# Kernel tuning notes

Measured on AMD Instinct MI355X. Metric: run time of the kernel, lower is better.

Reference implementation:

```python
import jax, jax.numpy as jnp
import numpy as np

B, S, D, H, FFN = 4, 1024, 1024, 16, 4096
DH = D // H
EPS = 1e-5
NEG = -1e20


def _layer_norm(t, g, b):
    m = jnp.mean(t, axis=-1, keepdims=True)
    v = jnp.mean((t - m) ** 2, axis=-1, keepdims=True)
    return (t - m) / jnp.sqrt(v + EPS) * g + b


def setup_inputs() -> dict:
    key = jax.random.key(0)
    ks = jax.random.split(key, 16)
    std_attn = np.sqrt(2.0 / (D + D)).astype(np.float32)  # xavier normal
    lim1 = np.sqrt(6.0 / (D + FFN)).astype(np.float32)    # xavier uniform
    inp = {
        'tensor': jax.random.normal(ks[0], (B, S, D), jnp.float32),
        'mask': jnp.ones((B, S), jnp.int32),
        'wq': jax.random.normal(ks[1], (D, D), jnp.float32) * std_attn,
        'bq': jnp.zeros((D,), jnp.float32),
        'wk': jax.random.normal(ks[2], (D, D), jnp.float32) * std_attn,
        'bk': jnp.zeros((D,), jnp.float32),
        'wv': jax.random.normal(ks[3], (D, D), jnp.float32) * std_attn,
        'bv': jnp.zeros((D,), jnp.float32),
        'wo': jax.random.normal(ks[4], (D, D), jnp.float32) * std_attn,
        'bo': jnp.zeros((D,), jnp.float32),
        'ln1_g': jnp.ones((D,), jnp.float32),
        'ln1_b': jnp.zeros((D,), jnp.float32),
        'w1': jax.random.uniform(ks[5], (FFN, D), jnp.float32, -lim1, lim1),
        'b1': jnp.zeros((FFN,), jnp.float32),
        'w2': jax.random.uniform(ks[6], (D, FFN), jnp.float32, -lim1, lim1),
        'b2': jnp.zeros((D,), jnp.float32),
        'ln2_g': jnp.ones((D,), jnp.float32),
        'ln2_b': jnp.zeros((D,), jnp.float32),
    }
    return inp


def reference(tensor, mask, wq, bq, wk, bk, wv, bv, wo, bo,
              ln1_g, ln1_b, w1, b1, w2, b2, ln2_g, ln2_b):
    x = tensor
    scale = jnp.sqrt(jnp.float32(DH))
    # QKV projections -> [B, S, H, DH]
    q = (x @ wq.T + bq).reshape(B, S, H, DH)
    k = (x @ wk.T + bk).reshape(B, S, H, DH)
    v = (x @ wv.T + bv).reshape(B, S, H, DH)
    # scores [B, H, Sq, Sk]
    scores = jnp.einsum('bqhd,bkhd->bhqk', q / scale, k)
    blocked = (mask == 0)[:, None, None, :]  # True -> block
    scores = jnp.where(blocked, NEG, scores)
    attn = jax.nn.softmax(scores.astype(jnp.float32), axis=-1).astype(x.dtype)
    ctx = jnp.einsum('bhqk,bkhd->bqhd', attn, v).reshape(B, S, D)
    attn_out = ctx @ wo.T + bo
    # post-LN (variant='aiayn')
    t = _layer_norm(x + attn_out, ln1_g, ln1_b)
    ffn = jax.nn.relu(t @ w1.T + b1) @ w2.T + b2
    t = _layer_norm(t + ffn, ln2_g, ln2_b)
    t = t * mask[:, :, None].astype(t.dtype)
    return t
```

## Files before the change

kernel.cpp:

```cpp
#include <hip/hip_runtime.h>

typedef __bf16 bf16x8 __attribute__((ext_vector_type(8)));
typedef __bf16 bf16x4 __attribute__((ext_vector_type(4)));
typedef float f32x4 __attribute__((ext_vector_type(4)));
typedef float f32x16 __attribute__((ext_vector_type(16)));

#define BB 4
#define SS 1024
#define DD 1024
#define HH 16
#define DHH 64
#define FFN 4096

__device__ __forceinline__ void gload_lds16(const void* g, void* lds) {
  __builtin_amdgcn_global_load_lds(
      (const __attribute__((address_space(1))) unsigned int*)g,
      (__attribute__((address_space(3))) unsigned int*)lds, 16, 0, 0);
}

__global__ __launch_bounds__(256) void cvt_all_kernel(
    const float* __restrict__ x, const float* __restrict__ wq, const float* __restrict__ wk,
    const float* __restrict__ wv, const float* __restrict__ wo, const float* __restrict__ w1,
    const float* __restrict__ w2, __bf16* __restrict__ xb, __bf16* __restrict__ wqkvb,
    __bf16* __restrict__ wob, __bf16* __restrict__ w1b, __bf16* __restrict__ w2b)
{
  int i = blockIdx.x * 256 + threadIdx.x;
  const float* src; __bf16* dst; int off;
  if (i < 524288)       { src = x;  dst = xb;              off = i; }
  else if (i < 655360)  { src = wq; dst = wqkvb;           off = i - 524288; }
  else if (i < 786432)  { src = wk; dst = wqkvb + 1048576; off = i - 655360; }
  else if (i < 917504)  { src = wv; dst = wqkvb + 2097152; off = i - 786432; }
  else if (i < 1048576) { src = wo; dst = wob;             off = i - 917504; }
  else if (i < 1572864) { src = w1; dst = w1b;             off = i - 1048576; }
  else                  { src = w2; dst = w2b;             off = i - 1572864; }
  float4 a = *(const float4*)(src + off * 8);
  float4 b = *(const float4*)(src + off * 8 + 4);
  bf16x8 v;
  v[0] = (__bf16)a.x; v[1] = (__bf16)a.y; v[2] = (__bf16)a.z; v[3] = (__bf16)a.w;
  v[4] = (__bf16)b.x; v[5] = (__bf16)b.y; v[6] = (__bf16)b.z; v[7] = (__bf16)b.w;
  *(bf16x8*)(dst + off * 8) = v;
}

template<int MODE>
__global__ __launch_bounds__(256, 2) void gemm_bt(
    const __bf16* __restrict__ A, const __bf16* __restrict__ Bw,
    const float* __restrict__ bias, const float* __restrict__ bias1, const float* __restrict__ bias2,
    const float* __restrict__ res, void* __restrict__ outp, void* __restrict__ out1,
    int M, int N, int K, int kLen, float scale)
{
  __shared__ __bf16 As[2][128 * 32];
  __shared__ __bf16 Bs[2][128 * 32];
  const int tid = threadIdx.x;
  const int wid = tid >> 6;
  const int lane = tid & 63;
  const int lr = lane & 15;
  const int lg = lane >> 4;

  const int gx = gridDim.x;
  const int nwg = gx * gridDim.y;
  const int wg = blockIdx.y * gx + blockIdx.x;
  const int swz = (wg & 7) * (nwg >> 3) + (wg >> 3);
  const int bm = (swz / gx) * 128;
  const int bn = (swz % gx) * 128;

  const int wm = (wid >> 1) * 64;
  const int wn = (wid & 1) * 64;

  int kBeg = 0, nk = K >> 5;
  if constexpr (MODE == 5) { kBeg = blockIdx.z * kLen; nk = kLen >> 5; }

  const int off = tid * 16;
  const int srow = off >> 6;
  const int scol = (off & 63) >> 1;
  const __bf16* gA0 = A + (size_t)(bm + srow) * K + kBeg + scol;
  const __bf16* gA1 = A + (size_t)(bm + 64 + srow) * K + kBeg + scol;
  const __bf16* gB0 = Bw + (size_t)(bn + srow) * K + kBeg + scol;
  const __bf16* gB1 = Bw + (size_t)(bn + 64 + srow) * K + kBeg + scol;
  char* lA = (char*)&As[0][0] + wid * 1024;
  char* lB = (char*)&Bs[0][0] + wid * 1024;

  f32x4 acc[4][4] = {};

#define STAGE(buf, kk) do { \
    gload_lds16(gA0 + (kk), lA + (buf) * 8192); \
    gload_lds16(gA1 + (kk), lA + (buf) * 8192 + 4096); \
    gload_lds16(gB0 + (kk), lB + (buf) * 8192); \
    gload_lds16(gB1 + (kk), lB + (buf) * 8192 + 4096); \
  } while (0)

  STAGE(0, 0);
  __syncthreads();
  for (int t = 0; t < nk; ++t) {
    const int cur = t & 1;
    if (t + 1 < nk) STAGE(cur ^ 1, (t + 1) << 5);
    bf16x8 af[4], bv[4];
#pragma unroll
    for (int i = 0; i < 4; ++i)
      af[i] = *(const bf16x8*)&As[cur][(wm + i * 16 + lr) * 32 + lg * 8];
#pragma unroll
    for (int i = 0; i < 4; ++i)
      bv[i] = *(const bf16x8*)&Bs[cur][(wn + i * 16 + lr) * 32 + lg * 8];
#pragma unroll
    for (int i = 0; i < 4; ++i)
#pragma unroll
      for (int j = 0; j < 4; ++j)
        acc[i][j] = __builtin_amdgcn_mfma_f32_16x16x32_bf16(af[i], bv[j], acc[i][j], 0, 0, 0);
    __syncthreads();
  }
#undef STAGE

#pragma unroll
  for (int i = 0; i < 4; ++i) {
#pragma unroll
    for (int j = 0; j < 4; ++j) {
#pragma unroll
      for (int r = 0; r < 4; ++r) {
        int row = bm + wm + i * 16 + lg * 4 + r;
        int col = bn + wn + j * 16 + lr;
        float v = acc[i][j][r];
        if constexpr (MODE == 2) {
          size_t idx = (size_t)row * N + col;
          ((float*)outp)[idx] = v + bias[col] + res[idx];
        } else if constexpr (MODE == 3) {
          float t2 = v + bias[col];
          ((__bf16*)outp)[(size_t)row * N + col] = (__bf16)fmaxf(t2, 0.f);
        } else if constexpr (MODE == 4) {
          int region = col >> 10;
          int col_ = col & 1023;
          int b_ = row >> 10, s_ = row & 1023;
          int h_ = col_ >> 6, d_ = col_ & 63;
          if (region == 0) {
            float v2 = (v + bias[col_]) * scale;
            ((__bf16*)outp)[(((size_t)(b_ * HH + h_) * SS) + s_) * DHH + d_] = (__bf16)v2;
          } else if (region == 1) {
            float v2 = v + bias1[col_];
            ((__bf16*)out1)[(((size_t)(b_ * HH + h_) * SS) + s_) * DHH + d_] = (__bf16)v2;
          } else {
            float v2 = v + bias2[col_];
            ((__bf16*)res)[(((size_t)(b_ * HH + h_) * DHH) + d_) * SS + s_] = (__bf16)v2;
          }
        } else {
          float* dst = blockIdx.z ? (float*)out1 : (float*)outp;
          dst[(size_t)row * N + col] = v;
        }
      }
    }
  }
}

__global__ __launch_bounds__(256, 2) void attn_kernel(
    const __bf16* __restrict__ q, const __bf16* __restrict__ k,
    const __bf16* __restrict__ vt, const int* __restrict__ mask,
    __bf16* __restrict__ ctx)
{
  const int nwg = gridDim.x;
  const int wg = blockIdx.x;
  const int swzb = (wg & 7) * (nwg >> 3) + (wg >> 3);
  const int bh = swzb >> 3;
  const int qb = (swzb & 7) << 7;
  const int b = bh >> 4;

  const int tid = threadIdx.x, wid = tid >> 6, lane = tid & 63;
  const int ln = lane & 31, hi = lane >> 5;

  __shared__ __bf16 Kt[2][64 * 64];
  __shared__ __bf16 Vt[2][64 * 64];
  __shared__ __bf16 Pt[4][32 * 64];
  __shared__ float mmulLds[SS];

  {
    const int* mrow = mask + b * SS;
    int c = tid * 4;
    float4 mm;
    mm.x = (float)(mrow[c + 0] != 0);
    mm.y = (float)(mrow[c + 1] != 0);
    mm.z = (float)(mrow[c + 2] != 0);
    mm.w = (float)(mrow[c + 3] != 0);
    ((float4*)mmulLds)[tid] = mm;
  }

  const __bf16* qh = q + (size_t)bh * SS * DHH;
  const __bf16* kh = k + (size_t)bh * SS * DHH;
  const __bf16* vh = vt + (size_t)bh * DHH * SS;

  const int qw = qb + wid * 32;
  bf16x8 qf[4];
#pragma unroll
  for (int s = 0; s < 4; ++s)
    qf[s] = *(const bf16x8*)&qh[(size_t)(qw + ln) * DHH + s * 16 + hi * 8];

  const int srow = tid >> 3;
  const int ps = tid & 7;
  const int sw0 = (srow ^ (srow >> 3)) & 7;
  const int r1 = srow + 32;
  const int sw1 = (r1 ^ (r1 >> 3)) & 7;
  const __bf16* kS0 = kh + (size_t)srow * DHH + ((ps ^ sw0) * 8);
  const __bf16* kS1 = kh + (size_t)r1 * DHH + ((ps ^ sw1) * 8);
  const __bf16* vS0 = vh + (size_t)srow * SS + ((ps ^ sw0) * 8);
  const __bf16* vS1 = vh + (size_t)r1 * SS + ((ps ^ sw1) * 8);

#define ASTAGE(bufi, kb_) do { \
    gload_lds16(kS0 + (size_t)(kb_) * DHH, (char*)&Kt[bufi][0] + wid * 1024); \
    gload_lds16(kS1 + (size_t)(kb_) * DHH, (char*)&Kt[bufi][0] + wid * 1024 + 4096); \
    gload_lds16(vS0 + (kb_), (char*)&Vt[bufi][0] + wid * 1024); \
    gload_lds16(vS1 + (kb_), (char*)&Vt[bufi][0] + wid * 1024 + 4096); \
  } while (0)

  char* Pw = (char*)&Pt[wid][0];
  const int swA = (ln ^ (ln >> 3)) & 7;
  const int swB = swA ^ 4;

  f32x16 o0 = {}, o1 = {};
  float l[16];
#pragma unroll
  for (int r = 0; r < 16; ++r) l[r] = 0.f;

  ASTAGE(0, 0);
  __syncthreads();

#pragma unroll 1
  for (int t = 0; t < SS / 64; ++t) {
    const int cur = t & 1;
    const int kb = t * 64;
    if (t + 1 < SS / 64) ASTAGE(cur ^ 1, kb + 64);

    const char* Kc = (const char*)&Kt[cur][0];
    const char* Vc = (const char*)&Vt[cur][0];

    f32x16 sc0 = {}, sc1 = {};
#pragma unroll
    for (int s = 0; s < 4; ++s) {
      bf16x8 kb0 = *(const bf16x8*)(Kc + ln * 128 + (((s * 2 + hi) ^ swA) << 4));
      bf16x8 kb1 = *(const bf16x8*)(Kc + (32 + ln) * 128 + (((s * 2 + hi) ^ swB) << 4));
      sc0 = __builtin_amdgcn_mfma_f32_32x32x16_bf16(qf[s], kb0, sc0, 0, 0, 0);
      sc1 = __builtin_amdgcn_mfma_f32_32x32x16_bf16(qf[s], kb1, sc1, 0, 0, 0);
    }

    float mm0 = mmulLds[kb + ln];
    float mm1 = mmulLds[kb + 32 + ln];
#pragma unroll
    for (int r = 0; r < 16; ++r) {
      float p0 = exp2f(sc0[r] - 23.0831207f) * mm0;
      float p1 = exp2f(sc1[r] - 23.0831207f) * mm1;
      l[r] += p0 + p1;
      int qrow = (r & 3) + 8 * (r >> 2) + 4 * hi;
      int swq = (qrow ^ (qrow >> 3)) & 7;
      *(__bf16*)(Pw + qrow * 128 + ((((ln >> 3) + 0) ^ swq) << 4) + (ln & 7) * 2) = (__bf16)p0;
      *(__bf16*)(Pw + qrow * 128 + ((((ln >> 3) + 4) ^ swq) << 4) + (ln & 7) * 2) = (__bf16)p1;
    }

#pragma unroll
    for (int ks = 0; ks < 4; ++ks) {
      bf16x8 pa = *(const bf16x8*)(Pw + ln * 128 + (((ks * 2 + hi) ^ swA) << 4));
      bf16x8 vb0 = *(const bf16x8*)(Vc + ln * 128 + (((ks * 2 + hi) ^ swA) << 4));
      bf16x8 vb1 = *(const bf16x8*)(Vc + (32 + ln) * 128 + (((ks * 2 + hi) ^ swB) << 4));
      o0 = __builtin_amdgcn_mfma_f32_32x32x16_bf16(pa, vb0, o0, 0, 0, 0);
      o1 = __builtin_amdgcn_mfma_f32_32x32x16_bf16(pa, vb1, o1, 0, 0, 0);
    }
    __syncthreads();
  }
#undef ASTAGE

#pragma unroll
  for (int r = 0; r < 16; ++r) {
#pragma unroll
    for (int off = 1; off < 32; off <<= 1) l[r] += __shfl_xor(l[r], off);
  }

#pragma unroll
  for (int r = 0; r < 16; ++r) {
    float inv = l[r] > 0.f ? 1.f / l[r] : 0.f;
    int qrow = (r & 3) + 8 * (r >> 2) + 4 * hi;
    size_t base = ((size_t)b * SS + qw + qrow) * DD + (size_t)(bh & 15) * DHH;
    ctx[base + ln] = (__bf16)(o0[r] * inv);
    ctx[base + 32 + ln] = (__bf16)(o1[r] * inv);
  }
}

__global__ __launch_bounds__(256) void ln_kernel(
    const float* __restrict__ in, const float* __restrict__ g, const float* __restrict__ b,
    float* __restrict__ out32, __bf16* __restrict__ out16)
{
  int row = blockIdx.x;
  int tid = threadIdx.x;
  int wid = tid >> 6, lane = tid & 63;
  float4 v = ((const float4*)(in + (size_t)row * DD))[tid];
  float s = v.x + v.y + v.z + v.w;
  float sq = v.x * v.x + v.y * v.y + v.z * v.z + v.w * v.w;
#pragma unroll
  for (int o = 1; o < 64; o <<= 1) { s += __shfl_xor(s, o); sq += __shfl_xor(sq, o); }
  __shared__ float red[8];
  if (lane == 0) { red[wid] = s; red[4 + wid] = sq; }
  __syncthreads();
  s = red[0] + red[1] + red[2] + red[3];
  sq = red[4] + red[5] + red[6] + red[7];
  float mean = s * (1.f / DD);
  float var = sq * (1.f / DD) - mean * mean;
  float rstd = rsqrtf(var + 1e-5f);
  float4 gg = ((const float4*)g)[tid];
  float4 bb = ((const float4*)b)[tid];
  float4 o;
  o.x = (v.x - mean) * rstd * gg.x + bb.x;
  o.y = (v.y - mean) * rstd * gg.y + bb.y;
  o.z = (v.z - mean) * rstd * gg.z + bb.z;
  o.w = (v.w - mean) * rstd * gg.w + bb.w;
  if (out32) ((float4*)(out32 + (size_t)row * DD))[tid] = o;
  if (out16) {
    bf16x4 w;
    w[0] = (__bf16)o.x; w[1] = (__bf16)o.y; w[2] = (__bf16)o.z; w[3] = (__bf16)o.w;
    *(bf16x4*)(out16 + (size_t)row * DD + tid * 4) = w;
  }
}

__global__ __launch_bounds__(256) void ln2_fused_kernel(
    const float* __restrict__ p0, const float* __restrict__ p1, const float* __restrict__ bias,
    const float* __restrict__ res, const float* __restrict__ g, const float* __restrict__ b,
    const int* __restrict__ mask, float* __restrict__ out)
{
  int row = blockIdx.x;
  int tid = threadIdx.x;
  int wid = tid >> 6, lane = tid & 63;
  size_t base = (size_t)row * DD;
  float4 a0 = ((const float4*)(p0 + base))[tid];
  float4 a1 = ((const float4*)(p1 + base))[tid];
  float4 rr = ((const float4*)(res + base))[tid];
  float4 bs = ((const float4*)bias)[tid];
  float4 v;
  v.x = a0.x + a1.x + rr.x + bs.x;
  v.y = a0.y + a1.y + rr.y + bs.y;
  v.z = a0.z + a1.z + rr.z + bs.z;
  v.w = a0.w + a1.w + rr.w + bs.w;
  float s = v.x + v.y + v.z + v.w;
  float sq = v.x * v.x + v.y * v.y + v.z * v.z + v.w * v.w;
#pragma unroll
  for (int o = 1; o < 64; o <<= 1) { s += __shfl_xor(s, o); sq += __shfl_xor(sq, o); }
  __shared__ float red[8];
  if (lane == 0) { red[wid] = s; red[4 + wid] = sq; }
  __syncthreads();
  s = red[0] + red[1] + red[2] + red[3];
  sq = red[4] + red[5] + red[6] + red[7];
  float mean = s * (1.f / DD);
  float var = sq * (1.f / DD) - mean * mean;
  float rstd = rsqrtf(var + 1e-5f);
  float4 gg = ((const float4*)g)[tid];
  float4 bb = ((const float4*)b)[tid];
  float mk = (float)mask[row];
  float4 o;
  o.x = ((v.x - mean) * rstd * gg.x + bb.x) * mk;
  o.y = ((v.y - mean) * rstd * gg.y + bb.y) * mk;
  o.z = ((v.z - mean) * rstd * gg.z + bb.z) * mk;
  o.w = ((v.w - mean) * rstd * gg.w + bb.w) * mk;
  ((float4*)(out + base))[tid] = o;
}

extern "C" void kernel_launch(void* const* d_in, const int* in_sizes, int n_in,
                              void* d_out, int out_size, void* d_ws, size_t ws_size,
                              hipStream_t stream) {
  const float* x    = (const float*)d_in[0];
  const int*  mask  = (const int*)d_in[1];
  const float* wq   = (const float*)d_in[2];
  const float* bq   = (const float*)d_in[3];
  const float* wk   = (const float*)d_in[4];
  const float* bk   = (const float*)d_in[5];
  const float* wv   = (const float*)d_in[6];
  const float* bv   = (const float*)d_in[7];
  const float* wo   = (const float*)d_in[8];
  const float* bo   = (const float*)d_in[9];
  const float* ln1g = (const float*)d_in[10];
  const float* ln1b = (const float*)d_in[11];
  const float* w1   = (const float*)d_in[12];
  const float* b1   = (const float*)d_in[13];
  const float* w2   = (const float*)d_in[14];
  const float* b2   = (const float*)d_in[15];
  const float* ln2g = (const float*)d_in[16];
  const float* ln2b = (const float*)d_in[17];
  float* out = (float*)d_out;
  char* ws = (char*)d_ws;

  __bf16* xb    = (__bf16*)(ws + 0);
  __bf16* wqkvb = (__bf16*)(ws + 8388608);
  __bf16* wob   = (__bf16*)(ws + 14680064);
  __bf16* w1b   = (__bf16*)(ws + 16777216);
  __bf16* w2b   = (__bf16*)(ws + 25165824);
  __bf16* qbuf  = (__bf16*)(ws + 33554432);
  __bf16* kbuf  = (__bf16*)(ws + 41943040);
  __bf16* vtbf  = (__bf16*)(ws + 50331648);
  __bf16* ctxb  = (__bf16*)(ws + 58720256);
  __bf16* hb    = (__bf16*)(ws + 33554432);
  float*  r1    = (float*)(ws + 67108864);
  float*  t32   = (float*)(ws + 83886080);
  __bf16* tb    = (__bf16*)(ws + 100663296);
  float*  p0    = r1;
  float*  p1    = (float*)(ws + 0);

  const int MSD = BB * SS;

  cvt_all_kernel<<<8192, 256, 0, stream>>>(x, wq, wk, wv, wo, w1, w2, xb, wqkvb, wob, w1b, w2b);

  gemm_bt<4><<<dim3(24, 32), 256, 0, stream>>>(xb, wqkvb, bq, bk, bv, (const float*)vtbf,
                                               qbuf, kbuf, MSD, 3072, DD, 0, 0.18033688f);

  attn_kernel<<<BB * HH * (SS / 128), 256, 0, stream>>>(qbuf, kbuf, vtbf, mask, ctxb);

  gemm_bt<2><<<dim3(8, 32), 256, 0, stream>>>(ctxb, wob, bo, nullptr, nullptr, x,
                                              r1, nullptr, MSD, DD, DD, 0, 1.0f);
  ln_kernel<<<MSD, 256, 0, stream>>>(r1, ln1g, ln1b, t32, tb);

  gemm_bt<3><<<dim3(32, 32), 256, 0, stream>>>(tb, w1b, b1, nullptr, nullptr, nullptr,
                                               hb, nullptr, MSD, FFN, DD, 0, 1.0f);
  gemm_bt<5><<<dim3(8, 32, 2), 256, 0, stream>>>(hb, w2b, nullptr, nullptr, nullptr, nullptr,
                                                 p0, p1, MSD, DD, FFN, 2048, 1.0f);
  ln2_fused_kernel<<<MSD, 256, 0, stream>>>(p0, p1, b2, t32, ln2g, ln2b, mask, out);
}
```

Before: 235.8 us.

## Add 4-stage pipelined 256-wide GEMM with swizzled LDS for QKV and FFN

```diff
diff --git a/kernel.cpp b/kernel.cpp
--- a/kernel.cpp
+++ b/kernel.cpp
@@ -41,87 +41,100 @@
   *(bf16x8*)(dst + off * 8) = v;
 }
 
-template<int MODE>
-__global__ __launch_bounds__(256, 2) void gemm_bt(
+template<int BM, int MODE>
+__global__ __launch_bounds__(512, 2) void gemm_pipe(
     const __bf16* __restrict__ A, const __bf16* __restrict__ Bw,
-    const float* __restrict__ bias, const float* __restrict__ bias1, const float* __restrict__ bias2,
-    const float* __restrict__ res, void* __restrict__ outp, void* __restrict__ out1,
+    const float* __restrict__ bias, const float* __restrict__ bias1,
+    const float* __restrict__ bias2, const float* __restrict__ res,
+    void* __restrict__ outp, void* __restrict__ out1,
     int M, int N, int K, int kLen, float scale)
 {
-  __shared__ __bf16 As[2][128 * 32];
-  __shared__ __bf16 Bs[2][128 * 32];
+  constexpr int MREP = BM / 32;
+  constexpr int ASLOT = BM * 64;
+  constexpr int BSLOT = 16384;
+  __shared__ char As[4 * ASLOT];
+  __shared__ char Bs[4 * BSLOT];
+
   const int tid = threadIdx.x;
-  const int wid = tid >> 6;
-  const int lane = tid & 63;
-  const int lr = lane & 15;
-  const int lg = lane >> 4;
+  const int wid = tid >> 6, lane = tid & 63;
+  const int lr = lane & 15, lg = lane >> 4;
+  const int wm = wid >> 2, wn = wid & 3;
 
   const int gx = gridDim.x;
   const int nwg = gx * gridDim.y;
   const int wg = blockIdx.y * gx + blockIdx.x;
   const int swz = (wg & 7) * (nwg >> 3) + (wg >> 3);
-  const int bm = (swz / gx) * 128;
-  const int bn = (swz % gx) * 128;
-
-  const int wm = (wid >> 1) * 64;
-  const int wn = (wid & 1) * 64;
-
-  int kBeg = 0, nk = K >> 5;
-  if constexpr (MODE == 5) { kBeg = blockIdx.z * kLen; nk = kLen >> 5; }
-
-  const int off = tid * 16;
-  const int srow = off >> 6;
-  const int scol = (off & 63) >> 1;
+  const int bm = (swz / gx) * BM;
+  const int bn = (swz % gx) * 256;
+
+  int kBeg = 0, KK = K;
+  if constexpr (MODE == 5) { kBeg = blockIdx.z * kLen; KK = kLen; }
+  const int NK = KK >> 5;
+
+  const int srow = tid >> 2;
+  const int scol = (((tid & 3) ^ ((srow >> 1) & 3)) << 3);
   const __bf16* gA0 = A + (size_t)(bm + srow) * K + kBeg + scol;
-  const __bf16* gA1 = A + (size_t)(bm + 64 + srow) * K + kBeg + scol;
+  const __bf16* gA1 = A + (size_t)(bm + 128 + srow) * K + kBeg + scol;
   const __bf16* gB0 = Bw + (size_t)(bn + srow) * K + kBeg + scol;
-  const __bf16* gB1 = Bw + (size_t)(bn + 64 + srow) * K + kBeg + scol;
-  char* lA = (char*)&As[0][0] + wid * 1024;
-  char* lB = (char*)&Bs[0][0] + wid * 1024;
-
-  f32x4 acc[4][4] = {};
-
-#define STAGE(buf, kk) do { \
-    gload_lds16(gA0 + (kk), lA + (buf) * 8192); \
-    gload_lds16(gA1 + (kk), lA + (buf) * 8192 + 4096); \
-    gload_lds16(gB0 + (kk), lB + (buf) * 8192); \
-    gload_lds16(gB1 + (kk), lB + (buf) * 8192 + 4096); \
+  const __bf16* gB1 = Bw + (size_t)(bn + 128 + srow) * K + kBeg + scol;
+  char* lA = As + wid * 1024;
+  char* lB = Bs + wid * 1024;
+
+  f32x4 acc[MREP][4] = {};
+
+#define STG(sI, kt) do { const int kk_ = (kt) << 5; \
+    gload_lds16(gA0 + kk_, lA + (sI) * ASLOT); \
+    if constexpr (BM == 256) gload_lds16(gA1 + kk_, lA + (sI) * ASLOT + 8192); \
+    gload_lds16(gB0 + kk_, lB + (sI) * BSLOT); \
+    gload_lds16(gB1 + kk_, lB + (sI) * BSLOT + 8192); \
   } while (0)
 
-  STAGE(0, 0);
-  __syncthreads();
-  for (int t = 0; t < nk; ++t) {
-    const int cur = t & 1;
-    if (t + 1 < nk) STAGE(cur ^ 1, (t + 1) << 5);
-    bf16x8 af[4], bv[4];
-#pragma unroll
-    for (int i = 0; i < 4; ++i)
-      af[i] = *(const bf16x8*)&As[cur][(wm + i * 16 + lr) * 32 + lg * 8];
-#pragma unroll
-    for (int i = 0; i < 4; ++i)
-      bv[i] = *(const bf16x8*)&Bs[cur][(wn + i * 16 + lr) * 32 + lg * 8];
-#pragma unroll
-    for (int i = 0; i < 4; ++i)
+  STG(0, 0); STG(1, 1); STG(2, 2);
+
+  const int swzb = (lg ^ ((lr >> 1) & 3)) << 4;
+
+#pragma unroll 1
+  for (int t = 0; t < NK; ++t) {
+    if constexpr (BM == 256)
+      asm volatile("s_waitcnt vmcnt(8)" ::: "memory");
+    else
+      asm volatile("s_waitcnt vmcnt(6)" ::: "memory");
+    __builtin_amdgcn_s_barrier();
+    __builtin_amdgcn_sched_barrier(0);
+    {
+      const int kt = (t + 3 < NK) ? (t + 3) : (NK - 1);
+      STG((t + 3) & 3, kt);
+    }
+    const char* Ac = As + (t & 3) * ASLOT;
+    const char* Bc = Bs + (t & 3) * BSLOT;
+    bf16x8 af[MREP], bf[4];
+#pragma unroll
+    for (int i = 0; i < MREP; ++i)
+      af[i] = *(const bf16x8*)(Ac + (wm * (BM / 2) + i * 16 + lr) * 64 + swzb);
+#pragma unroll
+    for (int j = 0; j < 4; ++j)
+      bf[j] = *(const bf16x8*)(Bc + (wn * 64 + j * 16 + lr) * 64 + swzb);
+    __builtin_amdgcn_s_setprio(1);
+#pragma unroll
+    for (int i = 0; i < MREP; ++i)
 #pragma unroll
       for (int j = 0; j < 4; ++j)
-        acc[i][j] = __builtin_amdgcn_mfma_f32_16x16x32_bf16(af[i], bv[j], acc[i][j], 0, 0, 0);
-    __syncthreads();
-  }
-#undef STAGE
-
-#pragma unroll
-  for (int i = 0; i < 4; ++i) {
+        acc[i][j] = __builtin_amdgcn_mfma_f32_16x16x32_bf16(af[i], bf[j], acc[i][j], 0, 0, 0);
+    __builtin_amdgcn_s_setprio(0);
+  }
+#undef STG
+  asm volatile("s_waitcnt vmcnt(0)" ::: "memory");
+
+#pragma unroll
+  for (int i = 0; i < MREP; ++i) {
 #pragma unroll
     for (int j = 0; j < 4; ++j) {
 #pragma unroll
       for (int r = 0; r < 4; ++r) {
-        int row = bm + wm + i * 16 + lg * 4 + r;
-        int col = bn + wn + j * 16 + lr;
+        int row = bm + wm * (BM / 2) + i * 16 + lg * 4 + r;
+        int col = bn + wn * 64 + j * 16 + lr;
         float v = acc[i][j][r];
-        if constexpr (MODE == 2) {
-          size_t idx = (size_t)row * N + col;
-          ((float*)outp)[idx] = v + bias[col] + res[idx];
-        } else if constexpr (MODE == 3) {
+        if constexpr (MODE == 3) {
           float t2 = v + bias[col];
           ((__bf16*)outp)[(size_t)row * N + col] = (__bf16)fmaxf(t2, 0.f);
         } else if constexpr (MODE == 4) {
@@ -148,6 +161,89 @@
   }
 }
 
+template<int MODE>
+__global__ __launch_bounds__(256, 2) void gemm_bt(
+    const __bf16* __restrict__ A, const __bf16* __restrict__ Bw,
+    const float* __restrict__ bias, const float* __restrict__ res,
+    void* __restrict__ outp, int M, int N, int K, float scale)
+{
+  __shared__ __bf16 As[2][128 * 32];
+  __shared__ __bf16 Bs[2][128 * 32];
+  const int tid = threadIdx.x;
+  const int wid = tid >> 6;
+  const int lane = tid & 63;
+  const int lr = lane & 15;
+  const int lg = lane >> 4;
+
+  const int gx = gridDim.x;
+  const int nwg = gx * gridDim.y;
+  const int wg = blockIdx.y * gx + blockIdx.x;
+  const int swz = (wg & 7) * (nwg >> 3) + (wg >> 3);
+  const int bm = (swz / gx) * 128;
+  const int bn = (swz % gx) * 128;
+
+  const int wm = (wid >> 1) * 64;
+  const int wn = (wid & 1) * 64;
+
+  const int off = tid * 16;
+  const int srow = off >> 6;
+  const int scol = (off & 63) >> 1;
+  const __bf16* gA0 = A + (size_t)(bm + srow) * K + scol;
+  const __bf16* gA1 = A + (size_t)(bm + 64 + srow) * K + scol;
+  const __bf16* gB0 = Bw + (size_t)(bn + srow) * K + scol;
+  const __bf16* gB1 = Bw + (size_t)(bn + 64 + srow) * K + scol;
+  char* lA = (char*)&As[0][0] + wid * 1024;
+  char* lB = (char*)&Bs[0][0] + wid * 1024;
+
+  f32x4 acc[4][4] = {};
+
+#define STAGE(buf, kk) do { \
+    gload_lds16(gA0 + (kk), lA + (buf) * 8192); \
+    gload_lds16(gA1 + (kk), lA + (buf) * 8192 + 4096); \
+    gload_lds16(gB0 + (kk), lB + (buf) * 8192); \
+    gload_lds16(gB1 + (kk), lB + (buf) * 8192 + 4096); \
+  } while (0)
+
+  STAGE(0, 0);
+  __syncthreads();
+  const int nk = K >> 5;
+  for (int t = 0; t < nk; ++t) {
+    const int cur = t & 1;
+    if (t + 1 < nk) STAGE(cur ^ 1, (t + 1) << 5);
+    bf16x8 af[4], bv[4];
+#pragma unroll
+    for (int i = 0; i < 4; ++i)
+      af[i] = *(const bf16x8*)&As[cur][(wm + i * 16 + lr) * 32 + lg * 8];
+#pragma unroll
+    for (int i = 0; i < 4; ++i)
+      bv[i] = *(const bf16x8*)&Bs[cur][(wn + i * 16 + lr) * 32 + lg * 8];
+#pragma unroll
+    for (int i = 0; i < 4; ++i)
+#pragma unroll
+      for (int j = 0; j < 4; ++j)
+        acc[i][j] = __builtin_amdgcn_mfma_f32_16x16x32_bf16(af[i], bv[j], acc[i][j], 0, 0, 0);
+    __syncthreads();
+  }
+#undef STAGE
+
+#pragma unroll
+  for (int i = 0; i < 4; ++i) {
+#pragma unroll
+    for (int j = 0; j < 4; ++j) {
+#pragma unroll
+      for (int r = 0; r < 4; ++r) {
+        int row = bm + wm + i * 16 + lg * 4 + r;
+        int col = bn + wn + j * 16 + lr;
+        float v = acc[i][j][r];
+        if constexpr (MODE == 2) {
+          size_t idx = (size_t)row * N + col;
+          ((float*)outp)[idx] = v + bias[col] + res[idx];
+        }
+      }
+    }
+  }
+}
+
 __global__ __launch_bounds__(256, 2) void attn_kernel(
     const __bf16* __restrict__ q, const __bf16* __restrict__ k,
     const __bf16* __restrict__ vt, const int* __restrict__ mask,
@@ -397,18 +493,19 @@
 
   cvt_all_kernel<<<8192, 256, 0, stream>>>(x, wq, wk, wv, wo, w1, w2, xb, wqkvb, wob, w1b, w2b);
 
-  gemm_bt<4><<<dim3(24, 32), 256, 0, stream>>>(xb, wqkvb, bq, bk, bv, (const float*)vtbf,
-                                               qbuf, kbuf, MSD, 3072, DD, 0, 0.18033688f);
+  gemm_pipe<256, 4><<<dim3(12, 16), 512, 0, stream>>>(
+      xb, wqkvb, bq, bk, bv, (const float*)vtbf, qbuf, kbuf, MSD, 3072, DD, 0, 0.18033688f);
 
   attn_kernel<<<BB * HH * (SS / 128), 256, 0, stream>>>(qbuf, kbuf, vtbf, mask, ctxb);
 
-  gemm_bt<2><<<dim3(8, 32), 256, 0, stream>>>(ctxb, wob, bo, nullptr, nullptr, x,
-                                              r1, nullptr, MSD, DD, DD, 0, 1.0f);
+  gemm_bt<2><<<dim3(8, 32), 256, 0, stream>>>(ctxb, wob, bo, x, r1, MSD, DD, DD, 1.0f);
   ln_kernel<<<MSD, 256, 0, stream>>>(r1, ln1g, ln1b, t32, tb);
 
-  gemm_bt<3><<<dim3(32, 32), 256, 0, stream>>>(tb, w1b, b1, nullptr, nullptr, nullptr,
-                                               hb, nullptr, MSD, FFN, DD, 0, 1.0f);
-  gemm_bt<5><<<dim3(8, 32, 2), 256, 0, stream>>>(hb, w2b, nullptr, nullptr, nullptr, nullptr,
-                                                 p0, p1, MSD, DD, FFN, 2048, 1.0f);
+  gemm_pipe<256, 3><<<dim3(16, 16), 512, 0, stream>>>(
+      tb, w1b, b1, nullptr, nullptr, nullptr, hb, nullptr, MSD, FFN, DD, 0, 1.0f);
+
+  gemm_pipe<128, 5><<<dim3(4, 32, 2), 512, 0, stream>>>(
+      hb, w2b, nullptr, nullptr, nullptr, nullptr, p0, p1, MSD, DD, FFN, 2048, 1.0f);
+
   ln2_fused_kernel<<<MSD, 256, 0, stream>>>(p0, p1, b2, t32, ln2g, ln2b, mask, out);
 }
```

Measured after the change: 289.3 us. +22.7%, slower.

## Add 256x256-tile 4-stage pipelined GEMM for the FFN up-projection

Applied to the files above, without the earlier changes.

```diff
diff --git a/kernel.cpp b/kernel.cpp
--- a/kernel.cpp
+++ b/kernel.cpp
@@ -42,6 +42,111 @@
 }
 
 template<int MODE>
+__global__ __launch_bounds__(512, 2) void gemm_r4(
+    const __bf16* __restrict__ Ag, const __bf16* __restrict__ Bg,
+    const float* __restrict__ bias, void* __restrict__ outp,
+    int M, int N, int K)
+{
+  __shared__ __bf16 LdsEl[65536];
+  char* L = (char*)LdsEl;
+  const int tid = threadIdx.x, wid = tid >> 6, lane = tid & 63;
+  const int wm = wid >> 2, wn = wid & 3, bh = wn >> 1;
+  const int lr = lane & 15, lg = lane >> 4;
+
+  const int gx = gridDim.x, nwg = gx * gridDim.y;
+  const int wg = blockIdx.y * gx + blockIdx.x;
+  const int swz = (wg & 7) * (nwg >> 3) + (wg >> 3);
+  const int bm = (swz / gx) * 256, bn = (swz % gx) * 256;
+
+  const int rowA0 = wn * 32;
+  const int rowB0 = (wn & 1) * 64 + wm * 32;
+  const __bf16* srcA[2]; const __bf16* srcB[2];
+#pragma unroll
+  for (int c = 0; c < 2; ++c) {
+    int ra = rowA0 + c * 16 + (lane >> 2);
+    srcA[c] = Ag + (size_t)(bm + wm * 128 + ra) * K + (((lane & 3) ^ (ra & 3)) << 3);
+    int rb = rowB0 + c * 16 + (lane >> 2);
+    srcB[c] = Bg + (size_t)(bn + bh * 128 + rb) * K + (((lane & 3) ^ (rb & 3)) << 3);
+  }
+  char* dA = L + wm * 8192 + rowA0 * 64;
+  char* dB = L + 65536 + bh * 8192 + rowB0 * 64;
+
+#define STGA(TAU, KT) do { \
+    gload_lds16(srcA[0] + (KT) * 32, dA + (TAU) * 16384); \
+    gload_lds16(srcA[1] + (KT) * 32, dA + (TAU) * 16384 + 1024); } while (0)
+#define STGB(TAU, KT) do { \
+    gload_lds16(srcB[0] + (KT) * 32, dB + (TAU) * 16384); \
+    gload_lds16(srcB[1] + (KT) * 32, dB + (TAU) * 16384 + 1024); } while (0)
+
+  f32x4 acc[8][4] = {};
+  const int NK = K >> 5;
+
+  STGA(0, 0); STGB(0, 0); STGA(1, 1); STGB(1, 1); STGA(2, 2); STGB(2, 2);
+
+  const int sA = (lg ^ (lr & 3)) << 4;
+
+#pragma unroll 1
+  for (int k = 0; k < NK; ++k) {
+    const int tau = k & 3;
+    const int kn = (k + 3 < NK) ? (k + 3) : (NK - 1);
+    const int tn = (k + 3) & 3;
+    asm volatile("s_waitcnt vmcnt(8)" ::: "memory");
+    __builtin_amdgcn_s_barrier();
+    __builtin_amdgcn_sched_barrier(0);
+    const char* Ac = L + (tau * 2 + wm) * 8192;
+    const char* Bc = L + 65536 + (tau * 2 + bh) * 8192;
+    bf16x8 bfr[4], af0[4], af1[4];
+#pragma unroll
+    for (int j = 0; j < 4; ++j)
+      bfr[j] = *(const bf16x8*)(Bc + ((wn & 1) * 64 + j * 16 + lr) * 64 + sA);
+#pragma unroll
+    for (int i = 0; i < 4; ++i)
+      af0[i] = *(const bf16x8*)(Ac + (i * 16 + lr) * 64 + sA);
+    STGA(tn, kn);
+    __builtin_amdgcn_s_barrier();
+    __builtin_amdgcn_s_setprio(1);
+#pragma unroll
+    for (int i = 0; i < 4; ++i)
+#pragma unroll
+      for (int j = 0; j < 4; ++j)
+        acc[i][j] = __builtin_amdgcn_mfma_f32_16x16x32_bf16(af0[i], bfr[j], acc[i][j], 0, 0, 0);
+    __builtin_amdgcn_s_setprio(0);
+#pragma unroll
+    for (int i = 0; i < 4; ++i)
+      af1[i] = *(const bf16x8*)(Ac + (64 + i * 16 + lr) * 64 + sA);
+    STGB(tn, kn);
+    __builtin_amdgcn_s_barrier();
+    __builtin_amdgcn_s_setprio(1);
+#pragma unroll
+    for (int i = 0; i < 4; ++i)
+#pragma unroll
+      for (int j = 0; j < 4; ++j)
+        acc[4 + i][j] = __builtin_amdgcn_mfma_f32_16x16x32_bf16(af1[i], bfr[j], acc[4 + i][j], 0, 0, 0);
+    __builtin_amdgcn_s_setprio(0);
+  }
+#undef STGA
+#undef STGB
+  asm volatile("s_waitcnt vmcnt(0)" ::: "memory");
+
+#pragma unroll
+  for (int ih = 0; ih < 2; ++ih)
+#pragma unroll
+    for (int i = 0; i < 4; ++i)
+#pragma unroll
+      for (int j = 0; j < 4; ++j)
+#pragma unroll
+        for (int r = 0; r < 4; ++r) {
+          int row = bm + wm * 128 + ih * 64 + i * 16 + lg * 4 + r;
+          int col = bn + wn * 64 + j * 16 + lr;
+          float v = acc[ih * 4 + i][j][r];
+          if constexpr (MODE == 3) {
+            float t2 = v + bias[col];
+            ((__bf16*)outp)[(size_t)row * N + col] = (__bf16)fmaxf(t2, 0.f);
+          }
+        }
+}
+
+template<int MODE>
 __global__ __launch_bounds__(256, 2) void gemm_bt(
     const __bf16* __restrict__ A, const __bf16* __restrict__ Bw,
     const float* __restrict__ bias, const float* __restrict__ bias1, const float* __restrict__ bias2,
@@ -121,9 +226,6 @@
         if constexpr (MODE == 2) {
           size_t idx = (size_t)row * N + col;
           ((float*)outp)[idx] = v + bias[col] + res[idx];
-        } else if constexpr (MODE == 3) {
-          float t2 = v + bias[col];
-          ((__bf16*)outp)[(size_t)row * N + col] = (__bf16)fmaxf(t2, 0.f);
         } else if constexpr (MODE == 4) {
           int region = col >> 10;
           int col_ = col & 1023;
@@ -139,7 +241,7 @@
             float v2 = v + bias2[col_];
             ((__bf16*)res)[(((size_t)(b_ * HH + h_) * DHH) + d_) * SS + s_] = (__bf16)v2;
           }
-        } else {
+        } else if constexpr (MODE == 5) {
           float* dst = blockIdx.z ? (float*)out1 : (float*)outp;
           dst[(size_t)row * N + col] = v;
         }
@@ -406,8 +508,8 @@
                                               r1, nullptr, MSD, DD, DD, 0, 1.0f);
   ln_kernel<<<MSD, 256, 0, stream>>>(r1, ln1g, ln1b, t32, tb);
 
-  gemm_bt<3><<<dim3(32, 32), 256, 0, stream>>>(tb, w1b, b1, nullptr, nullptr, nullptr,
-                                               hb, nullptr, MSD, FFN, DD, 0, 1.0f);
+  gemm_r4<3><<<dim3(16, 16), 512, 0, stream>>>(tb, w1b, b1, hb, MSD, FFN, DD);
+
   gemm_bt<5><<<dim3(8, 32, 2), 256, 0, stream>>>(hb, w2b, nullptr, nullptr, nullptr, nullptr,
                                                  p0, p1, MSD, DD, FFN, 2048, 1.0f);
   ln2_fused_kernel<<<MSD, 256, 0, stream>>>(p0, p1, b2, t32, ln2g, ln2b, mask, out);
```

Measured after the change: 232.5 us. Within noise of the previous version (-1.4%).

## Double GEMM K-tile to 64 with XOR-swizzled LDS layout

Applied to the files above, without the earlier changes.

```diff
diff --git a/kernel.cpp b/kernel.cpp
--- a/kernel.cpp
+++ b/kernel.cpp
@@ -48,13 +48,14 @@
     const float* __restrict__ res, void* __restrict__ outp, void* __restrict__ out1,
     int M, int N, int K, int kLen, float scale)
 {
-  __shared__ __bf16 As[2][128 * 32];
-  __shared__ __bf16 Bs[2][128 * 32];
+  __shared__ __bf16 As[2][128 * 64];
+  __shared__ __bf16 Bs[2][128 * 64];
   const int tid = threadIdx.x;
   const int wid = tid >> 6;
   const int lane = tid & 63;
   const int lr = lane & 15;
   const int lg = lane >> 4;
+  const int l7 = lr & 7;
 
   const int gx = gridDim.x;
   const int nwg = gx * gridDim.y;
@@ -66,45 +67,62 @@
   const int wm = (wid >> 1) * 64;
   const int wn = (wid & 1) * 64;
 
-  int kBeg = 0, nk = K >> 5;
-  if constexpr (MODE == 5) { kBeg = blockIdx.z * kLen; nk = kLen >> 5; }
-
-  const int off = tid * 16;
-  const int srow = off >> 6;
-  const int scol = (off & 63) >> 1;
-  const __bf16* gA0 = A + (size_t)(bm + srow) * K + kBeg + scol;
-  const __bf16* gA1 = A + (size_t)(bm + 64 + srow) * K + kBeg + scol;
-  const __bf16* gB0 = Bw + (size_t)(bn + srow) * K + kBeg + scol;
-  const __bf16* gB1 = Bw + (size_t)(bn + 64 + srow) * K + kBeg + scol;
+  int kBeg = 0, nk = K >> 6;
+  if constexpr (MODE == 5) { kBeg = blockIdx.z * kLen; nk = kLen >> 6; }
+
+  const int srow8 = tid >> 3;
+  const int ps = tid & 7;
+  const int swc = (ps ^ (srow8 & 7)) << 3;
+  const __bf16* gA0 = A + (size_t)(bm + srow8) * K + kBeg + swc;
+  const __bf16* gA1 = A + (size_t)(bm + 32 + srow8) * K + kBeg + swc;
+  const __bf16* gA2 = A + (size_t)(bm + 64 + srow8) * K + kBeg + swc;
+  const __bf16* gA3 = A + (size_t)(bm + 96 + srow8) * K + kBeg + swc;
+  const __bf16* gB0 = Bw + (size_t)(bn + srow8) * K + kBeg + swc;
+  const __bf16* gB1 = Bw + (size_t)(bn + 32 + srow8) * K + kBeg + swc;
+  const __bf16* gB2 = Bw + (size_t)(bn + 64 + srow8) * K + kBeg + swc;
+  const __bf16* gB3 = Bw + (size_t)(bn + 96 + srow8) * K + kBeg + swc;
   char* lA = (char*)&As[0][0] + wid * 1024;
   char* lB = (char*)&Bs[0][0] + wid * 1024;
 
   f32x4 acc[4][4] = {};
 
 #define STAGE(buf, kk) do { \
-    gload_lds16(gA0 + (kk), lA + (buf) * 8192); \
-    gload_lds16(gA1 + (kk), lA + (buf) * 8192 + 4096); \
-    gload_lds16(gB0 + (kk), lB + (buf) * 8192); \
-    gload_lds16(gB1 + (kk), lB + (buf) * 8192 + 4096); \
+    gload_lds16(gA0 + (kk), lA + (buf) * 16384); \
+    gload_lds16(gA1 + (kk), lA + (buf) * 16384 + 4096); \
+    gload_lds16(gA2 + (kk), lA + (buf) * 16384 + 8192); \
+    gload_lds16(gA3 + (kk), lA + (buf) * 16384 + 12288); \
+    gload_lds16(gB0 + (kk), lB + (buf) * 16384); \
+    gload_lds16(gB1 + (kk), lB + (buf) * 16384 + 4096); \
+    gload_lds16(gB2 + (kk), lB + (buf) * 16384 + 8192); \
+    gload_lds16(gB3 + (kk), lB + (buf) * 16384 + 12288); \
   } while (0)
 
   STAGE(0, 0);
   __syncthreads();
+  const char* Ab = (const char*)&As[0][0];
+  const char* Bb = (const char*)&Bs[0][0];
+  const int sl0 = ((0 * 4 + lg) ^ l7) << 4;
+  const int sl1 = ((1 * 4 + lg) ^ l7) << 4;
   for (int t = 0; t < nk; ++t) {
     const int cur = t & 1;
-    if (t + 1 < nk) STAGE(cur ^ 1, (t + 1) << 5);
-    bf16x8 af[4], bv[4];
-#pragma unroll
-    for (int i = 0; i < 4; ++i)
-      af[i] = *(const bf16x8*)&As[cur][(wm + i * 16 + lr) * 32 + lg * 8];
-#pragma unroll
-    for (int i = 0; i < 4; ++i)
-      bv[i] = *(const bf16x8*)&Bs[cur][(wn + i * 16 + lr) * 32 + lg * 8];
-#pragma unroll
-    for (int i = 0; i < 4; ++i)
-#pragma unroll
-      for (int j = 0; j < 4; ++j)
-        acc[i][j] = __builtin_amdgcn_mfma_f32_16x16x32_bf16(af[i], bv[j], acc[i][j], 0, 0, 0);
+    if (t + 1 < nk) STAGE(cur ^ 1, (t + 1) << 6);
+    bf16x8 af[2][4], bv[2][4];
+#pragma unroll
+    for (int i = 0; i < 4; ++i) {
+      int rowA = (wm + i * 16 + lr) << 7;
+      af[0][i] = *(const bf16x8*)(Ab + cur * 16384 + rowA + sl0);
+      af[1][i] = *(const bf16x8*)(Ab + cur * 16384 + rowA + sl1);
+      int rowB = (wn + i * 16 + lr) << 7;
+      bv[0][i] = *(const bf16x8*)(Bb + cur * 16384 + rowB + sl0);
+      bv[1][i] = *(const bf16x8*)(Bb + cur * 16384 + rowB + sl1);
+    }
+#pragma unroll
+    for (int ks = 0; ks < 2; ++ks)
+#pragma unroll
+      for (int i = 0; i < 4; ++i)
+#pragma unroll
+        for (int j = 0; j < 4; ++j)
+          acc[i][j] = __builtin_amdgcn_mfma_f32_16x16x32_bf16(af[ks][i], bv[ks][j], acc[i][j], 0, 0, 0);
     __syncthreads();
   }
 #undef STAGE
@@ -139,7 +157,7 @@
             float v2 = v + bias2[col_];
             ((__bf16*)res)[(((size_t)(b_ * HH + h_) * DHH) + d_) * SS + s_] = (__bf16)v2;
           }
-        } else {
+        } else if constexpr (MODE == 5) {
           float* dst = blockIdx.z ? (float*)out1 : (float*)outp;
           dst[(size_t)row * N + col] = v;
         }
@@ -408,6 +426,7 @@
 
   gemm_bt<3><<<dim3(32, 32), 256, 0, stream>>>(tb, w1b, b1, nullptr, nullptr, nullptr,
                                                hb, nullptr, MSD, FFN, DD, 0, 1.0f);
+
   gemm_bt<5><<<dim3(8, 32, 2), 256, 0, stream>>>(hb, w2b, nullptr, nullptr, nullptr, nullptr,
                                                  p0, p1, MSD, DD, FFN, 2048, 1.0f);
   ln2_fused_kernel<<<MSD, 256, 0, stream>>>(p0, p1, b2, t32, ln2g, ln2b, mask, out);
```

Result: slower. 247.2 us (+4.8%).
